# Performance work log

Hardware: AMD Instinct MI355X
Metric: run time of the kernel (lower is better)

## Reference

```python
import jax, jax.numpy as jnp
import numpy as np

NB_HEAD = 16
DIM_PER_HEAD = 64
EMB = 1024
B, SQ, SK = 4, 2048, 2048


def setup_inputs() -> dict:
    key = jax.random.key(0)
    ks = jax.random.split(key, 8)
    scale = 1.0 / np.sqrt(EMB)
    return {
        "hidden_state_query": jax.random.normal(ks[0], (B, SQ, EMB), jnp.float32),
        "hidden_state_key": jax.random.normal(ks[1], (B, SK, EMB), jnp.float32),
        "hidden_state_value": jax.random.normal(ks[2], (B, SK, EMB), jnp.float32),
        "attention_mask": jax.random.randint(ks[3], (B, SQ, SK), 0, 2).astype(bool),
        "Wq": jax.random.uniform(ks[4], (NB_HEAD * DIM_PER_HEAD, EMB), jnp.float32, -scale, scale),
        "Wk": jax.random.uniform(ks[5], (NB_HEAD * DIM_PER_HEAD, EMB), jnp.float32, -scale, scale),
        "Wv": jax.random.uniform(ks[6], (NB_HEAD * DIM_PER_HEAD, EMB), jnp.float32, -scale, scale),
        "Wo": jax.random.uniform(ks[7], (EMB, NB_HEAD * DIM_PER_HEAD), jnp.float32, -scale, scale),
    }


def reference(hidden_state_query, hidden_state_key, hidden_state_value,
              attention_mask, Wq, Wk, Wv, Wo):
    bs, sq, _ = hidden_state_query.shape
    sk = hidden_state_key.shape[1]
    # projections (nn.Linear without bias: x @ W.T)
    q = (hidden_state_query @ Wq.T).reshape(bs, sq, NB_HEAD, DIM_PER_HEAD).transpose(0, 2, 1, 3)
    k = (hidden_state_key @ Wk.T).reshape(bs, sk, NB_HEAD, DIM_PER_HEAD).transpose(0, 2, 1, 3)
    v = (hidden_state_value @ Wv.T).reshape(bs, sk, NB_HEAD, DIM_PER_HEAD).transpose(0, 2, 1, 3)
    scores = jnp.einsum('bhqd,bhkd->bhqk', q, k) / jnp.sqrt(jnp.asarray(DIM_PER_HEAD, q.dtype))
    attn = jax.nn.softmax(scores, axis=-1)
    # POST-softmax zero masking (True -> 0), broadcast over heads; no renormalization
    attn = jnp.where(attention_mask[:, None, :, :], jnp.asarray(0.0, attn.dtype), attn)
    ctx = jnp.einsum('bhqk,bhkd->bhqd', attn, v)  # [B,H,Sq,Dh]
    ctx = ctx.transpose(0, 2, 1, 3).reshape(bs, sq, NB_HEAD * DIM_PER_HEAD)
    return ctx @ Wo.T + hidden_state_query
```

## Files before the change

kernel.cpp:

```cpp
#include <hip/hip_runtime.h>
#include <hip/hip_bf16.h>
#include <stdint.h>

typedef __bf16 bf16_t;
typedef bf16_t bf16x2 __attribute__((ext_vector_type(2)));
typedef bf16_t bf16x8 __attribute__((ext_vector_type(8)));
typedef float  f32x4  __attribute__((ext_vector_type(4)));
typedef float  f32x16 __attribute__((ext_vector_type(16)));
typedef unsigned uint2v __attribute__((ext_vector_type(2)));

#define NB_HEAD 16
#define DH      64
#define EMB     1024
#define BATCH   4
#define SEQ     2048
#define NTOK    (BATCH*SEQ)

#define QSCALE 0.1803368801111204f

__device__ __forceinline__ void gload_lds16(const void* g, void* l) {
  __builtin_amdgcn_global_load_lds(
      (const __attribute__((address_space(1))) void*)g,
      (__attribute__((address_space(3))) void*)l, 16, 0, 0);
}

__device__ __forceinline__ uint32_t pkbf(float a, float b) {
  bf16x2 v = { (bf16_t)a, (bf16_t)b };
  return __builtin_bit_cast(uint32_t, v);
}

__device__ __forceinline__ void cvt8_body(const float* __restrict__ in,
                                          bf16_t* __restrict__ out, int i) {
  const float4* p = reinterpret_cast<const float4*>(in) + (size_t)i * 2;
  float4 a = p[0], b = p[1];
  uint4 r;
  r.x = pkbf(a.x, a.y); r.y = pkbf(a.z, a.w);
  r.z = pkbf(b.x, b.y); r.w = pkbf(b.z, b.w);
  reinterpret_cast<uint4*>(out)[i] = r;
}

__device__ __forceinline__ void mkand_body(const uint8_t* __restrict__ m,
                                           uint16_t* __restrict__ out, int i) {
  uint2 v = reinterpret_cast<const uint2*>(m)[i];
  uint4 r;
  uint32_t lo = v.x, hi = v.y;
  uint16_t e[8];
#pragma unroll
  for (int j = 0; j < 4; j++) e[j]     = (uint16_t)(((lo >> (8 * j)) & 0xFF) - 1);
#pragma unroll
  for (int j = 0; j < 4; j++) e[4 + j] = (uint16_t)(((hi >> (8 * j)) & 0xFF) - 1);
  r.x = (uint32_t)e[0] | ((uint32_t)e[1] << 16);
  r.y = (uint32_t)e[2] | ((uint32_t)e[3] << 16);
  r.z = (uint32_t)e[4] | ((uint32_t)e[5] << 16);
  r.w = (uint32_t)e[6] | ((uint32_t)e[7] << 16);
  reinterpret_cast<uint4*>(out)[i] = r;
}

__global__ void __launch_bounds__(256)
prep(const float* __restrict__ hq, const float* __restrict__ hk,
     const float* __restrict__ hv, const float* __restrict__ Wq,
     const float* __restrict__ Wk, const float* __restrict__ Wv,
     const float* __restrict__ Wo,
     bf16_t* hq_b, bf16_t* hk_b, bf16_t* hv_b,
     bf16_t* Wq_b, bf16_t* Wk_b, bf16_t* Wv_b, bf16_t* Wo_b,
     const uint8_t* __restrict__ mask, uint16_t* __restrict__ mand) {
  const int bid = blockIdx.x;
  if (bid < 12288) {
    const int seg = bid >> 12;
    const float* src = seg == 0 ? hq : seg == 1 ? hk : hv;
    bf16_t*      dst = seg == 0 ? hq_b : seg == 1 ? hk_b : hv_b;
    cvt8_body(src, dst, (bid & 4095) * 256 + (int)threadIdx.x);
  } else if (bid < 14336) {
    const int sb = bid - 12288;
    const int seg = sb >> 9;
    const float* src = seg == 0 ? Wq : seg == 1 ? Wk : seg == 2 ? Wv : Wo;
    bf16_t*      dst = seg == 0 ? Wq_b : seg == 1 ? Wk_b : seg == 2 ? Wv_b : Wo_b;
    cvt8_body(src, dst, (sb & 511) * 256 + (int)threadIdx.x);
  } else {
    mkand_body(mask, mand, (bid - 14336) * 256 + (int)threadIdx.x);
  }
}

__global__ void __launch_bounds__(256)
mkand(const uint8_t* __restrict__ m, uint16_t* __restrict__ out) {
  mkand_body(m, out, blockIdx.x * 256 + (int)threadIdx.x);
}

#define BM 128
#define BN 128
#define BKT 64

template<int EPI>
__global__ void __launch_bounds__(256, 2)
gemm_bt(const bf16_t* __restrict__ A, const bf16_t* __restrict__ Bw,
        bf16_t* __restrict__ Cb, float* __restrict__ Cf,
        const float* __restrict__ resid, float qscale) {
  __shared__ bf16_t As[2][BM * BKT];
  __shared__ bf16_t Bs[2][BN * BKT];
  const int K = EMB, N = EMB;
  const int t    = threadIdx.x;
  const int lane = t & 63, w = t >> 6;
  const int wr = w >> 1, wc = w & 1;
  const int l15 = lane & 15, l4 = lane >> 4;

  const int lin = blockIdx.x + 8 * blockIdx.y;
  const int nl  = (lin & 7) * 64 + (lin >> 3);
  const int rowBase = (nl >> 3) * BM, colBase = (nl & 7) * BN;

  f32x4 acc[4][4];
#pragma unroll
  for (int i = 0; i < 4; i++)
#pragma unroll
    for (int j = 0; j < 4; j++) acc[i][j] = f32x4{0.f, 0.f, 0.f, 0.f};

  const int lin16 = w * 1024 + lane * 16;

#pragma unroll
  for (int i = 0; i < 4; ++i) {
    int off  = i * 4096 + lin16;
    int row  = off >> 7, colb = off & 127;
    gload_lds16((const char*)A  + (((size_t)(rowBase + row)) * K) * 2 + colb, (char*)As[0] + off);
    gload_lds16((const char*)Bw + (((size_t)(colBase + row)) * K) * 2 + colb, (char*)Bs[0] + off);
  }
  __syncthreads();

  int cur = 0;
  for (int k0 = 0; k0 < K; k0 += BKT) {
    if (k0 + BKT < K) {
      const int nb = cur ^ 1;
#pragma unroll
      for (int i = 0; i < 4; ++i) {
        int off  = i * 4096 + lin16;
        int row  = off >> 7, colb = off & 127;
        gload_lds16((const char*)A  + (((size_t)(rowBase + row)) * K + k0 + BKT) * 2 + colb, (char*)As[nb] + off);
        gload_lds16((const char*)Bw + (((size_t)(colBase + row)) * K + k0 + BKT) * 2 + colb, (char*)Bs[nb] + off);
      }
    }
#pragma unroll
    for (int kc = 0; kc < 2; ++kc) {
      bf16x8 af[4], bfb[4];
#pragma unroll
      for (int mi = 0; mi < 4; mi++)
        af[mi] = *reinterpret_cast<const bf16x8*>(
            &As[cur][(wr * 64 + mi * 16 + l15) * BKT + kc * 32 + l4 * 8]);
#pragma unroll
      for (int ni = 0; ni < 4; ni++)
        bfb[ni] = *reinterpret_cast<const bf16x8*>(
            &Bs[cur][(wc * 64 + ni * 16 + l15) * BKT + kc * 32 + l4 * 8]);
      __builtin_amdgcn_s_setprio(1);
#pragma unroll
      for (int mi = 0; mi < 4; mi++)
#pragma unroll
        for (int ni = 0; ni < 4; ni++)
          acc[mi][ni] = __builtin_amdgcn_mfma_f32_16x16x32_bf16(
              af[mi], bfb[ni], acc[mi][ni], 0, 0, 0);
      __builtin_amdgcn_s_setprio(0);
    }
    __syncthreads();
    cur ^= 1;
  }

#pragma unroll
  for (int mi = 0; mi < 4; mi++) {
#pragma unroll
    for (int ni = 0; ni < 4; ni++) {
      const int m0 = rowBase + wr * 64 + mi * 16 + l4 * 4;
      const int n  = colBase + wc * 64 + ni * 16 + l15;
      if (EPI == 1) {
        const int bq = m0 >> 11, s0 = m0 & 2047, hh = n >> 6, d = n & 63;
        size_t local = (size_t)(s0 >> 6) * 4096 + ((s0 >> 4) & 3) * 1024 +
                       (d >> 5) * 512 + ((s0 >> 3) & 1) * 256 + (d & 31) * 8 + (s0 & 7);
        uint2 st;
        st.x = pkbf(acc[mi][ni][0], acc[mi][ni][1]);
        st.y = pkbf(acc[mi][ni][2], acc[mi][ni][3]);
        *reinterpret_cast<uint2*>(Cb + (size_t)(bq * 16 + hh) * 131072 + local) = st;
      } else {
#pragma unroll
        for (int r = 0; r < 4; r++) {
          int m = m0 + r;
          float v = acc[mi][ni][r];
          if (EPI == 0) {
            Cb[(size_t)m * N + n] = (bf16_t)(v * qscale);
          } else if (EPI == 3) {
            const int bq = m >> 11, s = m & 2047, hh = n >> 6, d = n & 63;
            size_t local = (size_t)(s >> 6) * 4096 + ((s >> 5) & 1) * 2048 +
                           (d >> 4) * 512 + ((d >> 3) & 1) * 256 + (s & 31) * 8 + (d & 7);
            Cb[(size_t)(bq * 16 + hh) * 131072 + local] = (bf16_t)v;
          } else {
            Cf[(size_t)m * N + n] = v + resid[(size_t)m * N + n];
          }
        }
      }
    }
  }
}

__global__ void __launch_bounds__(512, 2)
attn32(const bf16_t* __restrict__ Qb, const bf16_t* __restrict__ Kh,
       const bf16_t* __restrict__ Vt, const uint16_t* __restrict__ Mand,
       bf16_t* __restrict__ ctx) {
  __shared__ __align__(16) bf16_t Ks[2][64 * 64];
  __shared__ __align__(16) bf16_t Vs[2][64 * 64];

  const int t = threadIdx.x, lane = t & 63, wid = t >> 6;
  const int q = lane & 31, hi = lane >> 5;
  const int l16 = lane * 16;

  const int lin = blockIdx.x + 8 * (blockIdx.y + 16 * blockIdx.z);
  const int nl  = (lin & 7) * 64 + (lin >> 3);
  const int bx = nl & 7, h = (nl >> 3) & 15, b = nl >> 7;

  const int q0 = bx * 256 + wid * 32;
  const int qrow = b * SEQ + q0 + q;

  const char* kg = (const char*)(Kh + ((size_t)(b * NB_HEAD + h)) * SEQ * DH);
  const char* vg = (const char*)(Vt + ((size_t)(b * NB_HEAD + h)) * SEQ * DH);

  const bf16_t* qp = Qb + (size_t)qrow * EMB + h * DH + hi * 8;
  bf16x8 qf[4];
#pragma unroll
  for (int d = 0; d < 4; d++) qf[d] = *reinterpret_cast<const bf16x8*>(qp + d * 16);

  f32x16 o0 = {0}, o1 = {0};
  float lrun = 0.f;
  const uint16_t* mbase = Mand + (size_t)qrow * SEQ;

  gload_lds16(kg + t * 16, (char*)Ks[0] + t * 16);
  gload_lds16(vg + t * 16, (char*)Vs[0] + t * 16);
  __syncthreads();

  int cur = 0;
  for (int kb = 0; kb < SEQ; kb += 64) {
    if (kb + 64 < SEQ) {
      const int nb = cur ^ 1;
      gload_lds16(kg + (size_t)(kb + 64) * 128 + t * 16, (char*)Ks[nb] + t * 16);
      gload_lds16(vg + (size_t)(kb + 64) * 128 + t * 16, (char*)Vs[nb] + t * 16);
    }

    const char* kls = (const char*)Ks[cur];
    f32x16 p0 = {0}, p1 = {0};
    __builtin_amdgcn_s_setprio(1);
#pragma unroll
    for (int dsl = 0; dsl < 4; dsl++) {
      bf16x8 kf0 = *reinterpret_cast<const bf16x8*>(kls + dsl * 1024 + l16);
      bf16x8 kf1 = *reinterpret_cast<const bf16x8*>(kls + 4096 + dsl * 1024 + l16);
      p0 = __builtin_amdgcn_mfma_f32_32x32x16_bf16(kf0, qf[dsl], p0, 0, 0, 0);
      p1 = __builtin_amdgcn_mfma_f32_32x32x16_bf16(kf1, qf[dsl], p1, 0, 0, 0);
    }
    __builtin_amdgcn_s_setprio(0);

    uint4 mv[4];
#pragma unroll
    for (int ks = 0; ks < 4; ks++)
      mv[ks] = *reinterpret_cast<const uint4*>(mbase + kb + 16 * ks + 8 * hi);

    float ps = 0.f;
#pragma unroll
    for (int i = 0; i < 16; i++) { p0[i] = __builtin_amdgcn_exp2f(p0[i]); ps += p0[i]; }
#pragma unroll
    for (int i = 0; i < 16; i++) { p1[i] = __builtin_amdgcn_exp2f(p1[i]); ps += p1[i]; }
    ps += __shfl_xor(ps, 32);
    lrun += ps;

    const char* vls = (const char*)Vs[cur];
#pragma unroll
    for (int ks = 0; ks < 4; ks++) {
      const int s8 = (ks & 1) * 8;
      float e0, e1, e2, e3, e4, e5, e6, e7;
      if (ks < 2) {
        e0 = p0[s8+0]; e1 = p0[s8+1]; e2 = p0[s8+2]; e3 = p0[s8+3];
        e4 = p0[s8+4]; e5 = p0[s8+5]; e6 = p0[s8+6]; e7 = p0[s8+7];
      } else {
        e0 = p1[s8+0]; e1 = p1[s8+1]; e2 = p1[s8+2]; e3 = p1[s8+3];
        e4 = p1[s8+4]; e5 = p1[s8+5]; e6 = p1[s8+6]; e7 = p1[s8+7];
      }
      uint32_t a0 = pkbf(e0, e1), a1 = pkbf(e2, e3);
      uint32_t a2 = pkbf(e4, e5), a3 = pkbf(e6, e7);
      uint2v s02 = __builtin_amdgcn_permlane32_swap(a0, a2, false, false);
      uint2v s13 = __builtin_amdgcn_permlane32_swap(a1, a3, false, false);
      uint4 fr;
      fr.x = s02[0]; fr.y = s13[0]; fr.z = s02[1]; fr.w = s13[1];
      fr.x &= mv[ks].x; fr.y &= mv[ks].y; fr.z &= mv[ks].z; fr.w &= mv[ks].w;
      bf16x8 pa = __builtin_bit_cast(bf16x8, fr);
      bf16x8 vf0 = *reinterpret_cast<const bf16x8*>(vls + ks * 2048 + l16);
      bf16x8 vf1 = *reinterpret_cast<const bf16x8*>(vls + ks * 2048 + 1024 + l16);
      __builtin_amdgcn_s_setprio(1);
      o0 = __builtin_amdgcn_mfma_f32_32x32x16_bf16(vf0, pa, o0, 0, 0, 0);
      o1 = __builtin_amdgcn_mfma_f32_32x32x16_bf16(vf1, pa, o1, 0, 0, 0);
      __builtin_amdgcn_s_setprio(0);
    }

    __syncthreads();
    cur ^= 1;
  }

  float inv = 1.0f / lrun;
  bf16_t* cp = ctx + (size_t)qrow * EMB + h * DH;
#pragma unroll
  for (int g = 0; g < 4; g++) {
    uint2 st;
    st.x = pkbf(o0[4*g+0] * inv, o0[4*g+1] * inv);
    st.y = pkbf(o0[4*g+2] * inv, o0[4*g+3] * inv);
    *reinterpret_cast<uint2*>(cp + 8 * g + 4 * hi) = st;
    st.x = pkbf(o1[4*g+0] * inv, o1[4*g+1] * inv);
    st.y = pkbf(o1[4*g+2] * inv, o1[4*g+3] * inv);
    *reinterpret_cast<uint2*>(cp + 32 + 8 * g + 4 * hi) = st;
  }
}

extern "C" void kernel_launch(void* const* d_in, const int* in_sizes, int n_in,
                              void* d_out, int out_size, void* d_ws, size_t ws_size,
                              hipStream_t stream) {
  const float*   hq   = (const float*)d_in[0];
  const float*   hk   = (const float*)d_in[1];
  const float*   hv   = (const float*)d_in[2];
  const uint8_t* mask = (const uint8_t*)d_in[3];
  const float*   Wq   = (const float*)d_in[4];
  const float*   Wk   = (const float*)d_in[5];
  const float*   Wv   = (const float*)d_in[6];
  const float*   Wo   = (const float*)d_in[7];
  float* out = (float*)d_out;

  char* ws = (char*)d_ws;
  const size_t SZ_H = (size_t)NTOK * EMB * 2;
  const size_t SZ_W = (size_t)EMB * EMB * 2;
  bf16_t* hq_b = (bf16_t*)(ws + 0 * SZ_H);
  bf16_t* hk_b = (bf16_t*)(ws + 1 * SZ_H);
  bf16_t* hv_b = (bf16_t*)(ws + 2 * SZ_H);
  bf16_t* Qb   = (bf16_t*)(ws + 3 * SZ_H);
  bf16_t* Kh   = (bf16_t*)(ws + 4 * SZ_H);
  bf16_t* Vt   = (bf16_t*)(ws + 5 * SZ_H);
  bf16_t* ctx  = (bf16_t*)(ws + 6 * SZ_H);
  bf16_t* Wq_b = (bf16_t*)(ws + 7 * SZ_H + 0 * SZ_W);
  bf16_t* Wk_b = (bf16_t*)(ws + 7 * SZ_H + 1 * SZ_W);
  bf16_t* Wv_b = (bf16_t*)(ws + 7 * SZ_H + 2 * SZ_W);
  bf16_t* Wo_b = (bf16_t*)(ws + 7 * SZ_H + 3 * SZ_W);

  const size_t MAND_OFF = 7 * SZ_H + 4 * SZ_W;
  const size_t MAND_SZ  = (size_t)BATCH * SEQ * SEQ * 2;
  const bool bigws = ws_size >= MAND_OFF + MAND_SZ;
  uint16_t* Mand = bigws ? (uint16_t*)(ws + MAND_OFF) : (uint16_t*)ws;

  prep<<<bigws ? 22528 : 14336, 256, 0, stream>>>(
      hq, hk, hv, Wq, Wk, Wv, Wo,
      hq_b, hk_b, hv_b, Wq_b, Wk_b, Wv_b, Wo_b, mask, Mand);

  dim3 ggrid(EMB / BN, NTOK / BM);
  gemm_bt<0><<<ggrid, 256, 0, stream>>>(hq_b, Wq_b, Qb, nullptr, nullptr, QSCALE);
  gemm_bt<3><<<ggrid, 256, 0, stream>>>(hk_b, Wk_b, Kh, nullptr, nullptr, 1.0f);
  gemm_bt<1><<<ggrid, 256, 0, stream>>>(hv_b, Wv_b, Vt, nullptr, nullptr, 1.0f);

  if (!bigws) mkand<<<8192, 256, 0, stream>>>(mask, Mand);

  attn32<<<dim3(SEQ / 256, NB_HEAD, BATCH), 512, 0, stream>>>(Qb, Kh, Vt, Mand, ctx);

  gemm_bt<2><<<ggrid, 256, 0, stream>>>(ctx, Wo_b, nullptr, out, hq, 1.0f);
}
```

Baseline: 244.6 us.

## Fuse fp32-to-bf16 activation conversion into a single batched QKV GEMM

The separate conversion pass over the fp32 query/key/value activations is removed. A new gemm_qkv kernel loads fp32 rows directly, packs them to bf16 in registers and stores them to shared memory, and computes all three projections in one launch via blockIdx.z. The K tile is halved to 32 and the output GEMM gets a higher occupancy hint. The workspace layout is fixed, with the mask always converted in the prep kernel. This saves a full write and re-read of the bf16 activation copies and two kernel launches, at the cost of register-staged A loads instead of direct-to-LDS loads and more loop iterations with barriers.

```diff
diff --git a/kernel.cpp b/kernel.cpp
--- a/kernel.cpp
+++ b/kernel.cpp
@@ -57,44 +57,167 @@
 }
 
 __global__ void __launch_bounds__(256)
-prep(const float* __restrict__ hq, const float* __restrict__ hk,
-     const float* __restrict__ hv, const float* __restrict__ Wq,
-     const float* __restrict__ Wk, const float* __restrict__ Wv,
-     const float* __restrict__ Wo,
-     bf16_t* hq_b, bf16_t* hk_b, bf16_t* hv_b,
+prep(const float* __restrict__ Wq, const float* __restrict__ Wk,
+     const float* __restrict__ Wv, const float* __restrict__ Wo,
      bf16_t* Wq_b, bf16_t* Wk_b, bf16_t* Wv_b, bf16_t* Wo_b,
      const uint8_t* __restrict__ mask, uint16_t* __restrict__ mand) {
   const int bid = blockIdx.x;
-  if (bid < 12288) {
-    const int seg = bid >> 12;
-    const float* src = seg == 0 ? hq : seg == 1 ? hk : hv;
-    bf16_t*      dst = seg == 0 ? hq_b : seg == 1 ? hk_b : hv_b;
-    cvt8_body(src, dst, (bid & 4095) * 256 + (int)threadIdx.x);
-  } else if (bid < 14336) {
-    const int sb = bid - 12288;
-    const int seg = sb >> 9;
+  if (bid < 2048) {
+    const int seg = bid >> 9;
     const float* src = seg == 0 ? Wq : seg == 1 ? Wk : seg == 2 ? Wv : Wo;
     bf16_t*      dst = seg == 0 ? Wq_b : seg == 1 ? Wk_b : seg == 2 ? Wv_b : Wo_b;
-    cvt8_body(src, dst, (sb & 511) * 256 + (int)threadIdx.x);
+    cvt8_body(src, dst, (bid & 511) * 256 + (int)threadIdx.x);
   } else {
-    mkand_body(mask, mand, (bid - 14336) * 256 + (int)threadIdx.x);
-  }
-}
-
-__global__ void __launch_bounds__(256)
-mkand(const uint8_t* __restrict__ m, uint16_t* __restrict__ out) {
-  mkand_body(m, out, blockIdx.x * 256 + (int)threadIdx.x);
+    mkand_body(mask, mand, (bid - 2048) * 256 + (int)threadIdx.x);
+  }
 }
 
 #define BM 128
 #define BN 128
-#define BKT 64
-
-template<int EPI>
+#define BKT 32
+
 __global__ void __launch_bounds__(256, 2)
-gemm_bt(const bf16_t* __restrict__ A, const bf16_t* __restrict__ Bw,
-        bf16_t* __restrict__ Cb, float* __restrict__ Cf,
-        const float* __restrict__ resid, float qscale) {
+gemm_qkv(const float* __restrict__ hq, const float* __restrict__ hk,
+         const float* __restrict__ hv,
+         const bf16_t* __restrict__ Wq_b, const bf16_t* __restrict__ Wk_b,
+         const bf16_t* __restrict__ Wv_b,
+         bf16_t* __restrict__ Qb, bf16_t* __restrict__ Kf,
+         bf16_t* __restrict__ Vf) {
+  __shared__ bf16_t As[2][BM * BKT];
+  __shared__ bf16_t Bs[2][BN * BKT];
+  const int K = EMB;
+  const int z = blockIdx.z;
+  const float*  A  = z == 0 ? hq : z == 1 ? hk : hv;
+  const bf16_t* Bw = z == 0 ? Wq_b : z == 1 ? Wk_b : Wv_b;
+
+  const int t    = threadIdx.x;
+  const int lane = t & 63, w = t >> 6;
+  const int wr = w >> 1, wc = w & 1;
+  const int l15 = lane & 15, l4 = lane >> 4;
+
+  const int lin = blockIdx.x + 8 * blockIdx.y;
+  const int nl  = (lin & 7) * 64 + (lin >> 3);
+  const int rowBase = (nl >> 3) * BM, colBase = (nl & 7) * BN;
+
+  f32x4 acc[4][4];
+#pragma unroll
+  for (int i = 0; i < 4; i++)
+#pragma unroll
+    for (int j = 0; j < 4; j++) acc[i][j] = f32x4{0.f, 0.f, 0.f, 0.f};
+
+  const int t16 = t * 16;
+  const int ar = t >> 1, ac = (t & 1) * 16;
+  const float* arow = A + (size_t)(rowBase + ar) * K + ac;
+  char* const asdst0 = (char*)As[0] + ar * 64 + ac * 2;
+  char* const asdst1 = (char*)As[1] + ar * 64 + ac * 2;
+
+  {
+    float4 a0 = *reinterpret_cast<const float4*>(arow);
+    float4 a1 = *reinterpret_cast<const float4*>(arow + 4);
+    float4 a2 = *reinterpret_cast<const float4*>(arow + 8);
+    float4 a3 = *reinterpret_cast<const float4*>(arow + 12);
+#pragma unroll
+    for (int i = 0; i < 2; ++i) {
+      int off = i * 4096 + t16;
+      int row = off >> 6, colb = off & 63;
+      gload_lds16((const char*)Bw + (((size_t)(colBase + row)) * K) * 2 + colb, (char*)Bs[0] + off);
+    }
+    uint4 w0, w1;
+    w0.x = pkbf(a0.x, a0.y); w0.y = pkbf(a0.z, a0.w);
+    w0.z = pkbf(a1.x, a1.y); w0.w = pkbf(a1.z, a1.w);
+    w1.x = pkbf(a2.x, a2.y); w1.y = pkbf(a2.z, a2.w);
+    w1.z = pkbf(a3.x, a3.y); w1.w = pkbf(a3.z, a3.w);
+    *reinterpret_cast<uint4*>(asdst0) = w0;
+    *reinterpret_cast<uint4*>(asdst0 + 16) = w1;
+  }
+  __syncthreads();
+
+  int cur = 0;
+  for (int k0 = 0; k0 < K; k0 += BKT) {
+    float4 na0, na1, na2, na3;
+    const bool more = (k0 + BKT < K);
+    if (more) {
+      const float* ap = arow + k0 + BKT;
+      na0 = *reinterpret_cast<const float4*>(ap);
+      na1 = *reinterpret_cast<const float4*>(ap + 4);
+      na2 = *reinterpret_cast<const float4*>(ap + 8);
+      na3 = *reinterpret_cast<const float4*>(ap + 12);
+      const int nb = cur ^ 1;
+#pragma unroll
+      for (int i = 0; i < 2; ++i) {
+        int off = i * 4096 + t16;
+        int row = off >> 6, colb = off & 63;
+        gload_lds16((const char*)Bw + (((size_t)(colBase + row)) * K + k0 + BKT) * 2 + colb, (char*)Bs[nb] + off);
+      }
+    }
+    {
+      bf16x8 af[4], bfb[4];
+#pragma unroll
+      for (int mi = 0; mi < 4; mi++)
+        af[mi] = *reinterpret_cast<const bf16x8*>(
+            &As[cur][(wr * 64 + mi * 16 + l15) * BKT + l4 * 8]);
+#pragma unroll
+      for (int ni = 0; ni < 4; ni++)
+        bfb[ni] = *reinterpret_cast<const bf16x8*>(
+            &Bs[cur][(wc * 64 + ni * 16 + l15) * BKT + l4 * 8]);
+      __builtin_amdgcn_s_setprio(1);
+#pragma unroll
+      for (int mi = 0; mi < 4; mi++)
+#pragma unroll
+        for (int ni = 0; ni < 4; ni++)
+          acc[mi][ni] = __builtin_amdgcn_mfma_f32_16x16x32_bf16(
+              af[mi], bfb[ni], acc[mi][ni], 0, 0, 0);
+      __builtin_amdgcn_s_setprio(0);
+    }
+    if (more) {
+      uint4 w0, w1;
+      w0.x = pkbf(na0.x, na0.y); w0.y = pkbf(na0.z, na0.w);
+      w0.z = pkbf(na1.x, na1.y); w0.w = pkbf(na1.z, na1.w);
+      w1.x = pkbf(na2.x, na2.y); w1.y = pkbf(na2.z, na2.w);
+      w1.z = pkbf(na3.x, na3.y); w1.w = pkbf(na3.z, na3.w);
+      char* d = (cur ? asdst0 : asdst1);
+      *reinterpret_cast<uint4*>(d) = w0;
+      *reinterpret_cast<uint4*>(d + 16) = w1;
+    }
+    __syncthreads();
+    cur ^= 1;
+  }
+
+#pragma unroll
+  for (int mi = 0; mi < 4; mi++) {
+#pragma unroll
+    for (int ni = 0; ni < 4; ni++) {
+      const int m0 = rowBase + wr * 64 + mi * 16 + l4 * 4;
+      const int n  = colBase + wc * 64 + ni * 16 + l15;
+      if (z == 0) {
+#pragma unroll
+        for (int r = 0; r < 4; r++)
+          Qb[(size_t)(m0 + r) * EMB + n] = (bf16_t)(acc[mi][ni][r] * QSCALE);
+      } else if (z == 1) {
+#pragma unroll
+        for (int r = 0; r < 4; r++) {
+          int m = m0 + r;
+          const int bq = m >> 11, s = m & 2047, hh = n >> 6, d = n & 63;
+          size_t local = (size_t)(s >> 6) * 4096 + ((s >> 5) & 1) * 2048 +
+                         (d >> 4) * 512 + ((d >> 3) & 1) * 256 + (s & 31) * 8 + (d & 7);
+          Kf[(size_t)(bq * 16 + hh) * 131072 + local] = (bf16_t)acc[mi][ni][r];
+        }
+      } else {
+        const int bq = m0 >> 11, s0 = m0 & 2047, hh = n >> 6, d = n & 63;
+        size_t local = (size_t)(s0 >> 6) * 4096 + ((s0 >> 4) & 3) * 1024 +
+                       (d >> 5) * 512 + ((s0 >> 3) & 1) * 256 + (d & 31) * 8 + (s0 & 7);
+        uint2 st;
+        st.x = pkbf(acc[mi][ni][0], acc[mi][ni][1]);
+        st.y = pkbf(acc[mi][ni][2], acc[mi][ni][3]);
+        *reinterpret_cast<uint2*>(Vf + (size_t)(bq * 16 + hh) * 131072 + local) = st;
+      }
+    }
+  }
+}
+
+__global__ void __launch_bounds__(256, 4)
+gemm_out(const bf16_t* __restrict__ A, const bf16_t* __restrict__ Bw,
+         float* __restrict__ Cf, const float* __restrict__ resid) {
   __shared__ bf16_t As[2][BM * BKT];
   __shared__ bf16_t Bs[2][BN * BKT];
   const int K = EMB, N = EMB;
@@ -113,12 +236,12 @@
 #pragma unroll
     for (int j = 0; j < 4; j++) acc[i][j] = f32x4{0.f, 0.f, 0.f, 0.f};
 
-  const int lin16 = w * 1024 + lane * 16;
-
-#pragma unroll
-  for (int i = 0; i < 4; ++i) {
-    int off  = i * 4096 + lin16;
-    int row  = off >> 7, colb = off & 127;
+  const int t16 = t * 16;
+
+#pragma unroll
+  for (int i = 0; i < 2; ++i) {
+    int off = i * 4096 + t16;
+    int row = off >> 6, colb = off & 63;
     gload_lds16((const char*)A  + (((size_t)(rowBase + row)) * K) * 2 + colb, (char*)As[0] + off);
     gload_lds16((const char*)Bw + (((size_t)(colBase + row)) * K) * 2 + colb, (char*)Bs[0] + off);
   }
@@ -129,24 +252,23 @@
     if (k0 + BKT < K) {
       const int nb = cur ^ 1;
 #pragma unroll
-      for (int i = 0; i < 4; ++i) {
-        int off  = i * 4096 + lin16;
-        int row  = off >> 7, colb = off & 127;
+      for (int i = 0; i < 2; ++i) {
+        int off = i * 4096 + t16;
+        int row = off >> 6, colb = off & 63;
         gload_lds16((const char*)A  + (((size_t)(rowBase + row)) * K + k0 + BKT) * 2 + colb, (char*)As[nb] + off);
         gload_lds16((const char*)Bw + (((size_t)(colBase + row)) * K + k0 + BKT) * 2 + colb, (char*)Bs[nb] + off);
       }
     }
-#pragma unroll
-    for (int kc = 0; kc < 2; ++kc) {
+    {
       bf16x8 af[4], bfb[4];
 #pragma unroll
       for (int mi = 0; mi < 4; mi++)
         af[mi] = *reinterpret_cast<const bf16x8*>(
-            &As[cur][(wr * 64 + mi * 16 + l15) * BKT + kc * 32 + l4 * 8]);
+            &As[cur][(wr * 64 + mi * 16 + l15) * BKT + l4 * 8]);
 #pragma unroll
       for (int ni = 0; ni < 4; ni++)
         bfb[ni] = *reinterpret_cast<const bf16x8*>(
-            &Bs[cur][(wc * 64 + ni * 16 + l15) * BKT + kc * 32 + l4 * 8]);
+            &Bs[cur][(wc * 64 + ni * 16 + l15) * BKT + l4 * 8]);
       __builtin_amdgcn_s_setprio(1);
 #pragma unroll
       for (int mi = 0; mi < 4; mi++)
@@ -166,30 +288,10 @@
     for (int ni = 0; ni < 4; ni++) {
       const int m0 = rowBase + wr * 64 + mi * 16 + l4 * 4;
       const int n  = colBase + wc * 64 + ni * 16 + l15;
-      if (EPI == 1) {
-        const int bq = m0 >> 11, s0 = m0 & 2047, hh = n >> 6, d = n & 63;
-        size_t local = (size_t)(s0 >> 6) * 4096 + ((s0 >> 4) & 3) * 1024 +
-                       (d >> 5) * 512 + ((s0 >> 3) & 1) * 256 + (d & 31) * 8 + (s0 & 7);
-        uint2 st;
-        st.x = pkbf(acc[mi][ni][0], acc[mi][ni][1]);
-        st.y = pkbf(acc[mi][ni][2], acc[mi][ni][3]);
-        *reinterpret_cast<uint2*>(Cb + (size_t)(bq * 16 + hh) * 131072 + local) = st;
-      } else {
-#pragma unroll
-        for (int r = 0; r < 4; r++) {
-          int m = m0 + r;
-          float v = acc[mi][ni][r];
-          if (EPI == 0) {
-            Cb[(size_t)m * N + n] = (bf16_t)(v * qscale);
-          } else if (EPI == 3) {
-            const int bq = m >> 11, s = m & 2047, hh = n >> 6, d = n & 63;
-            size_t local = (size_t)(s >> 6) * 4096 + ((s >> 5) & 1) * 2048 +
-                           (d >> 4) * 512 + ((d >> 3) & 1) * 256 + (s & 31) * 8 + (d & 7);
-            Cb[(size_t)(bq * 16 + hh) * 131072 + local] = (bf16_t)v;
-          } else {
-            Cf[(size_t)m * N + n] = v + resid[(size_t)m * N + n];
-          }
-        }
+#pragma unroll
+      for (int r = 0; r < 4; r++) {
+        int m = m0 + r;
+        Cf[(size_t)m * N + n] = acc[mi][ni][r] + resid[(size_t)m * N + n];
       }
     }
   }
@@ -322,37 +424,24 @@
   float* out = (float*)d_out;
 
   char* ws = (char*)d_ws;
-  const size_t SZ_H = (size_t)NTOK * EMB * 2;
-  const size_t SZ_W = (size_t)EMB * EMB * 2;
-  bf16_t* hq_b = (bf16_t*)(ws + 0 * SZ_H);
-  bf16_t* hk_b = (bf16_t*)(ws + 1 * SZ_H);
-  bf16_t* hv_b = (bf16_t*)(ws + 2 * SZ_H);
-  bf16_t* Qb   = (bf16_t*)(ws + 3 * SZ_H);
-  bf16_t* Kh   = (bf16_t*)(ws + 4 * SZ_H);
-  bf16_t* Vt   = (bf16_t*)(ws + 5 * SZ_H);
-  bf16_t* ctx  = (bf16_t*)(ws + 6 * SZ_H);
-  bf16_t* Wq_b = (bf16_t*)(ws + 7 * SZ_H + 0 * SZ_W);
-  bf16_t* Wk_b = (bf16_t*)(ws + 7 * SZ_H + 1 * SZ_W);
-  bf16_t* Wv_b = (bf16_t*)(ws + 7 * SZ_H + 2 * SZ_W);
-  bf16_t* Wo_b = (bf16_t*)(ws + 7 * SZ_H + 3 * SZ_W);
-
-  const size_t MAND_OFF = 7 * SZ_H + 4 * SZ_W;
-  const size_t MAND_SZ  = (size_t)BATCH * SEQ * SEQ * 2;
-  const bool bigws = ws_size >= MAND_OFF + MAND_SZ;
-  uint16_t* Mand = bigws ? (uint16_t*)(ws + MAND_OFF) : (uint16_t*)ws;
-
-  prep<<<bigws ? 22528 : 14336, 256, 0, stream>>>(
-      hq, hk, hv, Wq, Wk, Wv, Wo,
-      hq_b, hk_b, hv_b, Wq_b, Wk_b, Wv_b, Wo_b, mask, Mand);
-
-  dim3 ggrid(EMB / BN, NTOK / BM);
-  gemm_bt<0><<<ggrid, 256, 0, stream>>>(hq_b, Wq_b, Qb, nullptr, nullptr, QSCALE);
-  gemm_bt<3><<<ggrid, 256, 0, stream>>>(hk_b, Wk_b, Kh, nullptr, nullptr, 1.0f);
-  gemm_bt<1><<<ggrid, 256, 0, stream>>>(hv_b, Wv_b, Vt, nullptr, nullptr, 1.0f);
-
-  if (!bigws) mkand<<<8192, 256, 0, stream>>>(mask, Mand);
-
-  attn32<<<dim3(SEQ / 256, NB_HEAD, BATCH), 512, 0, stream>>>(Qb, Kh, Vt, Mand, ctx);
-
-  gemm_bt<2><<<ggrid, 256, 0, stream>>>(ctx, Wo_b, nullptr, out, hq, 1.0f);
-}
+  const size_t MI = 1024 * 1024;
+  uint16_t* Mand = (uint16_t*)(ws);
+  bf16_t* Qb   = (bf16_t*)(ws + 32 * MI);
+  bf16_t* Kf   = (bf16_t*)(ws + 48 * MI);
+  bf16_t* Vf   = (bf16_t*)(ws + 64 * MI);
+  bf16_t* ctx  = (bf16_t*)(ws + 80 * MI);
+  bf16_t* Wq_b = (bf16_t*)(ws + 96 * MI);
+  bf16_t* Wk_b = (bf16_t*)(ws + 98 * MI);
+  bf16_t* Wv_b = (bf16_t*)(ws + 100 * MI);
+  bf16_t* Wo_b = (bf16_t*)(ws + 102 * MI);
+
+  prep<<<10240, 256, 0, stream>>>(Wq, Wk, Wv, Wo,
+                                  Wq_b, Wk_b, Wv_b, Wo_b, mask, Mand);
+
+  gemm_qkv<<<dim3(8, 64, 3), 256, 0, stream>>>(hq, hk, hv,
+                                               Wq_b, Wk_b, Wv_b, Qb, Kf, Vf);
+
+  attn32<<<dim3(SEQ / 256, NB_HEAD, BATCH), 512, 0, stream>>>(Qb, Kf, Vf, Mand, ctx);
+
+  gemm_out<<<dim3(8, 64), 256, 0, stream>>>(ctx, Wo_b, out, hq);
+}
```

Measured after the change: 245.6 us. About the same (+0.4%).
